# Kernel tuning notes

Measured on AMD Instinct MI355X. Metric: run time of the kernel, lower is better.

## Reference

```python
import jax, jax.numpy as jnp
import numpy as np

H = 1024      # LSTM_DIM
D = 1024      # BERT_DIM
VW = 30000    # word vocab
VA = 30       # action vocab
T = 64        # transition steps
S = 512       # BERT memory length


def lstm_cell(x, h, c, Wih, Whh, bih, bhh):
    # torch.nn.LSTMCell math: gates ordered i, f, g, o
    g = x @ Wih.T + bih + h @ Whh.T + bhh
    i, f, gg, o = jnp.split(g, 4, axis=-1)
    c2 = jax.nn.sigmoid(f) * c + jax.nn.sigmoid(i) * jnp.tanh(gg)
    h2 = jax.nn.sigmoid(o) * jnp.tanh(c2)
    return h2, c2


def forward(memory, actions, words,
            term_Wih, term_Whh, term_bih, term_bhh,
            act_Wih, act_Whh, act_bih, act_bhh,
            Wq, bq, Wa1, ba1, Wa2, ba2, Ww1, bw1, Ww2, bw2,
            act_emb, word_emb):
    z = jnp.zeros((1, H), dtype=memory.dtype)

    def step(carry, xs):
        term_h, term_c, act_h, act_c, stack_h = carry
        a_t, w_t = xs
        # predict_action: concat decoder states, dot-attention over BERT memory (no softmax)
        states = jnp.concatenate([term_h, act_h, stack_h], axis=1)     # [1, 3H]
        q = states @ Wq.T + bq                                          # [1, D]
        attn = jnp.einsum('bsd,bd->bs', memory, q)                      # [1, S]
        ctx = jnp.einsum('bs,bsd->bd', attn, memory)                    # [1, D]
        final = jnp.concatenate([states, ctx], axis=1)                  # [1, 3H+D]
        act_logits = jax.nn.relu(final @ Wa1.T + ba1) @ Wa2.T + ba2     # [1, VA]
        word_logits = jax.nn.relu(final @ Ww1.T + bw1) @ Ww2.T + bw2    # [1, VW]
        # do_action: act LSTM step, then SHIFT: word embedding into term LSTM + stack push
        a_e = act_emb[a_t][None, :]
        act_h2, act_c2 = lstm_cell(a_e, act_h, act_c, act_Wih, act_Whh, act_bih, act_bhh)
        w_e = word_emb[w_t][None, :]
        term_h2, term_c2 = lstm_cell(w_e, term_h, term_c, term_Wih, term_Whh, term_bih, term_bhh)
        new_carry = (term_h2, term_c2, act_h2, act_c2, w_e)
        return new_carry, (act_logits[0], word_logits[0])

    carry0 = (z, z, z, z, z)
    _, (act_logits, word_logits) = jax.lax.scan(step, carry0, (actions, words))
    return act_logits, word_logits  # [T, VA], [T, VW]


def setup_inputs() -> dict:
    key = jax.random.key(0)
    ks = jax.random.split(key, 24)
    s = 0.02

    def n(k, shape):
        return jax.random.normal(k, shape, dtype=jnp.float32) * s

    return {
        'memory': jax.random.normal(ks[0], (1, S, D), dtype=jnp.float32),
        'actions': jax.random.randint(ks[1], (T,), 0, VA),
        'words': jax.random.randint(ks[2], (T,), 0, VW),
        'term_Wih': n(ks[3], (4 * H, H)), 'term_Whh': n(ks[4], (4 * H, H)),
        'term_bih': n(ks[5], (4 * H,)), 'term_bhh': n(ks[6], (4 * H,)),
        'act_Wih': n(ks[7], (4 * H, H)), 'act_Whh': n(ks[8], (4 * H, H)),
        'act_bih': n(ks[9], (4 * H,)), 'act_bhh': n(ks[10], (4 * H,)),
        'Wq': n(ks[11], (D, 3 * H)), 'bq': n(ks[12], (D,)),
        'Wa1': n(ks[13], (H, 3 * H + D)), 'ba1': n(ks[14], (H,)),
        'Wa2': n(ks[15], (VA, H)), 'ba2': n(ks[16], (VA,)),
        'Ww1': n(ks[17], (H, 3 * H + D)), 'bw1': n(ks[18], (H,)),
        'Ww2': n(ks[19], (VW, H)), 'bw2': n(ks[20], (VW,)),
        'act_emb': n(ks[21], (VA, H)),
        'word_emb': n(ks[22], (VW, H)),
    }


def reference(memory, actions, words,
              term_Wih, term_Whh, term_bih, term_bhh,
              act_Wih, act_Whh, act_bih, act_bhh,
              Wq, bq, Wa1, ba1, Wa2, ba2, Ww1, bw1, Ww2, bw2,
              act_emb, word_emb):
    return forward(memory, actions, words,
                   term_Wih, term_Whh, term_bih, term_bhh,
                   act_Wih, act_Whh, act_bih, act_bhh,
                   Wq, bq, Wa1, ba1, Wa2, ba2, Ww1, bw1, Ww2, bw2,
                   act_emb, word_emb)
```

## Files before the change

kernel.cpp:

```cpp
#include <hip/hip_runtime.h>

#define H 1024
#define T_STEPS 64
#define S_MEM 512
#define VA 30
#define VW 30000

typedef unsigned long long u64;

__device__ __forceinline__ float sigmf(float x) { return 1.f / (1.f + expf(-x)); }

__global__ __launch_bounds__(256) void k_init(
    const int* __restrict__ actions, const int* __restrict__ words,
    const float* __restrict__ act_emb, const float* __restrict__ word_emb,
    float* __restrict__ X_term, float* __restrict__ X_act,
    float* __restrict__ fin, u64* __restrict__ htag) {
  int b = blockIdx.x, tid = threadIdx.x;
  if (b < T_STEPS) {
    int wi = words[b], ai = actions[b];
    for (int i = tid; i < H; i += 256) {
      float we = word_emb[(size_t)wi * H + i];
      X_term[b * H + i] = we;
      X_act[b * H + i]  = act_emb[(size_t)ai * H + i];
      if (b + 1 < T_STEPS) fin[(size_t)(b + 1) * 4096 + 2048 + i] = we;
    }
    if (b == 0)
      for (int i = tid; i < H; i += 256) fin[2048 + i] = 0.f;
  } else if (b == T_STEPS) {
    for (int i = tid; i < H; i += 256) { fin[i] = 0.f; fin[H + i] = 0.f; }
  } else {
    for (int i = (b - 65) * 256 + tid; i < 64 * 2048; i += 64 * 256) htag[i] = 0ull;
  }
}

__global__ __launch_bounds__(256) void k_gemm64(
    const float* __restrict__ A, int lda,
    const float* __restrict__ B, int ldb,
    int N, int K, float* __restrict__ Ppart) {
  __shared__ __align__(16) float As[64 * 64];
  __shared__ __align__(16) float Bs[64 * 64];
  const float4* As4 = (const float4*)As;
  const float4* Bs4 = (const float4*)Bs;
  int tid = threadIdx.x;
  int cidx = tid & 15;
  int ridx = tid >> 4;
  int n0 = blockIdx.x * 64;
  int klen = K / gridDim.y;
  int kbeg = blockIdx.y * klen;
  float acc[4][4] = {};

  for (int k0 = kbeg; k0 < kbeg + klen; k0 += 64) {
#pragma unroll
    for (int i = 0; i < 4; ++i) {
      int f = tid + i * 256;
      int rr = f >> 4, km = f & 15;
      float4 v = *(const float4*)&A[(size_t)rr * lda + k0 + km * 4];
      int c2 = ((rr >> 2) ^ km) & 15, p = rr & 3;
      As[(km * 4 + 0) * 64 + c2 * 4 + p] = v.x;
      As[(km * 4 + 1) * 64 + c2 * 4 + p] = v.y;
      As[(km * 4 + 2) * 64 + c2 * 4 + p] = v.z;
      As[(km * 4 + 3) * 64 + c2 * 4 + p] = v.w;
    }
#pragma unroll
    for (int i = 0; i < 4; ++i) {
      int f = tid + i * 256;
      int nn = f >> 4, km = f & 15;
      int gn = n0 + nn;
      float4 v = make_float4(0.f, 0.f, 0.f, 0.f);
      if (gn < N) v = *(const float4*)&B[(size_t)gn * ldb + k0 + km * 4];
      int c2 = ((nn >> 2) ^ km) & 15, p = nn & 3;
      Bs[(km * 4 + 0) * 64 + c2 * 4 + p] = v.x;
      Bs[(km * 4 + 1) * 64 + c2 * 4 + p] = v.y;
      Bs[(km * 4 + 2) * 64 + c2 * 4 + p] = v.z;
      Bs[(km * 4 + 3) * 64 + c2 * 4 + p] = v.w;
    }
    __syncthreads();
#pragma unroll 8
    for (int kk = 0; kk < 64; ++kk) {
      int sw = kk >> 2;
      float4 a4 = As4[kk * 16 + ((ridx ^ sw) & 15)];
      float4 b4 = Bs4[kk * 16 + ((cidx ^ sw) & 15)];
      float av[4] = {a4.x, a4.y, a4.z, a4.w};
      float bv[4] = {b4.x, b4.y, b4.z, b4.w};
#pragma unroll
      for (int i = 0; i < 4; ++i)
#pragma unroll
        for (int j = 0; j < 4; ++j) acc[i][j] += av[i] * bv[j];
    }
    __syncthreads();
  }

  int gcol = n0 + cidx * 4;
  float* P = Ppart + (size_t)blockIdx.y * 64 * N;
  if (gcol < N) {
#pragma unroll
    for (int i = 0; i < 4; ++i) {
      int row = ridx * 4 + i;
      *(float4*)&P[(size_t)row * N + gcol] =
          make_float4(acc[i][0], acc[i][1], acc[i][2], acc[i][3]);
    }
  }
}

__global__ __launch_bounds__(256) void k_gemm_dual(
    const float* __restrict__ A0, const float* __restrict__ A1, int lda,
    const float* __restrict__ B0, const float* __restrict__ B1, int ldb,
    int N, int K, float* __restrict__ P0, float* __restrict__ P1,
    const float* __restrict__ APc, int kb) {
  __shared__ __align__(16) float As[64 * 64];
  __shared__ __align__(16) float Bs[64 * 64];
  const float4* As4 = (const float4*)As;
  const float4* Bs4 = (const float4*)Bs;
  const float* A = blockIdx.z ? A1 : A0;
  const float* B = blockIdx.z ? B1 : B0;
  float* Pp = blockIdx.z ? P1 : P0;
  int tid = threadIdx.x;
  int cidx = tid & 15;
  int ridx = tid >> 4;
  int n0 = blockIdx.x * 64;
  int klen = K / gridDim.y;
  int kbeg = blockIdx.y * klen;
  float acc[4][4] = {};

  for (int k0 = kbeg; k0 < kbeg + klen; k0 += 64) {
#pragma unroll
    for (int i = 0; i < 4; ++i) {
      int f = tid + i * 256;
      int rr = f >> 4, km = f & 15;
      float4 v;
      if (k0 >= kb) {
        int kc = k0 - kb + km * 4;
        float4 a = *(const float4*)&APc[(size_t)rr * 1024 + kc];
        float4 c = *(const float4*)&APc[65536 + (size_t)rr * 1024 + kc];
        v = make_float4(a.x + c.x, a.y + c.y, a.z + c.z, a.w + c.w);
      } else {
        v = *(const float4*)&A[(size_t)rr * lda + k0 + km * 4];
      }
      int c2 = ((rr >> 2) ^ km) & 15, p = rr & 3;
      As[(km * 4 + 0) * 64 + c2 * 4 + p] = v.x;
      As[(km * 4 + 1) * 64 + c2 * 4 + p] = v.y;
      As[(km * 4 + 2) * 64 + c2 * 4 + p] = v.z;
      As[(km * 4 + 3) * 64 + c2 * 4 + p] = v.w;
    }
#pragma unroll
    for (int i = 0; i < 4; ++i) {
      int f = tid + i * 256;
      int nn = f >> 4, km = f & 15;
      int gn = n0 + nn;
      float4 v = make_float4(0.f, 0.f, 0.f, 0.f);
      if (gn < N) v = *(const float4*)&B[(size_t)gn * ldb + k0 + km * 4];
      int c2 = ((nn >> 2) ^ km) & 15, p = nn & 3;
      Bs[(km * 4 + 0) * 64 + c2 * 4 + p] = v.x;
      Bs[(km * 4 + 1) * 64 + c2 * 4 + p] = v.y;
      Bs[(km * 4 + 2) * 64 + c2 * 4 + p] = v.z;
      Bs[(km * 4 + 3) * 64 + c2 * 4 + p] = v.w;
    }
    __syncthreads();
#pragma unroll 8
    for (int kk = 0; kk < 64; ++kk) {
      int sw = kk >> 2;
      float4 a4 = As4[kk * 16 + ((ridx ^ sw) & 15)];
      float4 b4 = Bs4[kk * 16 + ((cidx ^ sw) & 15)];
      float av[4] = {a4.x, a4.y, a4.z, a4.w};
      float bv[4] = {b4.x, b4.y, b4.z, b4.w};
#pragma unroll
      for (int i = 0; i < 4; ++i)
#pragma unroll
        for (int j = 0; j < 4; ++j) acc[i][j] += av[i] * bv[j];
    }
    __syncthreads();
  }
  int gcol = n0 + cidx * 4;
  float* P = Pp + (size_t)blockIdx.y * 64 * N;
  if (gcol < N) {
#pragma unroll
    for (int i = 0; i < 4; ++i) {
      int row = ridx * 4 + i;
      *(float4*)&P[(size_t)row * N + gcol] =
          make_float4(acc[i][0], acc[i][1], acc[i][2], acc[i][3]);
    }
  }
}

__global__ __launch_bounds__(256) void k_attn(
    const float* __restrict__ Pq, const float* __restrict__ bq,
    const float* __restrict__ mem, float* __restrict__ Pa) {
  __shared__ __align__(16) float As[64 * 64];
  __shared__ __align__(16) float Bs[64 * 64];
  const float4* As4 = (const float4*)As;
  const float4* Bs4 = (const float4*)Bs;
  int tid = threadIdx.x;
  int cidx = tid & 15;
  int ridx = tid >> 4;
  int n0 = blockIdx.x * 64;
  int kbeg = blockIdx.y * 128;
  float acc[4][4] = {};

  for (int k0 = kbeg; k0 < kbeg + 128; k0 += 64) {
#pragma unroll
    for (int i = 0; i < 4; ++i) {
      int f = tid + i * 256;
      int rr = f >> 4, km = f & 15;
      int col = k0 + km * 4;
      float4 v = *(const float4*)&bq[col];
#pragma unroll
      for (int s = 0; s < 8; ++s) {
        float4 p = *(const float4*)&Pq[(size_t)s * 65536 + (size_t)rr * 1024 + col];
        v.x += p.x; v.y += p.y; v.z += p.z; v.w += p.w;
      }
      int c2 = ((rr >> 2) ^ km) & 15, p = rr & 3;
      As[(km * 4 + 0) * 64 + c2 * 4 + p] = v.x;
      As[(km * 4 + 1) * 64 + c2 * 4 + p] = v.y;
      As[(km * 4 + 2) * 64 + c2 * 4 + p] = v.z;
      As[(km * 4 + 3) * 64 + c2 * 4 + p] = v.w;
    }
#pragma unroll
    for (int i = 0; i < 4; ++i) {
      int f = tid + i * 256;
      int nn = f >> 4, km = f & 15;
      float4 v = *(const float4*)&mem[(size_t)(n0 + nn) * 1024 + k0 + km * 4];
      int c2 = ((nn >> 2) ^ km) & 15, p = nn & 3;
      Bs[(km * 4 + 0) * 64 + c2 * 4 + p] = v.x;
      Bs[(km * 4 + 1) * 64 + c2 * 4 + p] = v.y;
      Bs[(km * 4 + 2) * 64 + c2 * 4 + p] = v.z;
      Bs[(km * 4 + 3) * 64 + c2 * 4 + p] = v.w;
    }
    __syncthreads();
#pragma unroll 8
    for (int kk = 0; kk < 64; ++kk) {
      int sw = kk >> 2;
      float4 a4 = As4[kk * 16 + ((ridx ^ sw) & 15)];
      float4 b4 = Bs4[kk * 16 + ((cidx ^ sw) & 15)];
      float av[4] = {a4.x, a4.y, a4.z, a4.w};
      float bv[4] = {b4.x, b4.y, b4.z, b4.w};
#pragma unroll
      for (int i = 0; i < 4; ++i)
#pragma unroll
        for (int j = 0; j < 4; ++j) acc[i][j] += av[i] * bv[j];
    }
    __syncthreads();
  }
  int gcol = n0 + cidx * 4;
  float* P = Pa + (size_t)blockIdx.y * 64 * 512;
#pragma unroll
  for (int i = 0; i < 4; ++i) {
    int row = ridx * 4 + i;
    *(float4*)&P[(size_t)row * 512 + gcol] =
        make_float4(acc[i][0], acc[i][1], acc[i][2], acc[i][3]);
  }
}

__global__ __launch_bounds__(256) void k_ctx(
    const float* __restrict__ Pa, const float* __restrict__ mem,
    float* __restrict__ Pc) {
  __shared__ __align__(16) float As[64 * 64];
  __shared__ __align__(16) float Bs[64 * 64];
  const float4* As4 = (const float4*)As;
  const float4* Bs4 = (const float4*)Bs;
  int tid = threadIdx.x;
  int cidx = tid & 15;
  int ridx = tid >> 4;
  int n0 = blockIdx.x * 64;
  int kbeg = blockIdx.y * 256;
  float acc[4][4] = {};

  for (int k0 = kbeg; k0 < kbeg + 256; k0 += 64) {
#pragma unroll
    for (int i = 0; i < 4; ++i) {
      int f = tid + i * 256;
      int rr = f >> 4, km = f & 15;
      int col = k0 + km * 4;
      float4 v = make_float4(0.f, 0.f, 0.f, 0.f);
#pragma unroll
      for (int s = 0; s < 8; ++s) {
        float4 p = *(const float4*)&Pa[(size_t)s * 32768 + (size_t)rr * 512 + col];
        v.x += p.x; v.y += p.y; v.z += p.z; v.w += p.w;
      }
      int c2 = ((rr >> 2) ^ km) & 15, p = rr & 3;
      As[(km * 4 + 0) * 64 + c2 * 4 + p] = v.x;
      As[(km * 4 + 1) * 64 + c2 * 4 + p] = v.y;
      As[(km * 4 + 2) * 64 + c2 * 4 + p] = v.z;
      As[(km * 4 + 3) * 64 + c2 * 4 + p] = v.w;
    }
#pragma unroll
    for (int i = 0; i < 4; ++i) {
      int f = tid + i * 256;
      int kr = f >> 4, nq = f & 15;
      float4 v = *(const float4*)&mem[(size_t)(k0 + kr) * 1024 + n0 + nq * 4];
      ((float4*)Bs)[kr * 16 + ((nq ^ (kr >> 2)) & 15)] = v;
    }
    __syncthreads();
#pragma unroll 8
    for (int kk = 0; kk < 64; ++kk) {
      int sw = kk >> 2;
      float4 a4 = As4[kk * 16 + ((ridx ^ sw) & 15)];
      float4 b4 = Bs4[kk * 16 + ((cidx ^ sw) & 15)];
      float av[4] = {a4.x, a4.y, a4.z, a4.w};
      float bv[4] = {b4.x, b4.y, b4.z, b4.w};
#pragma unroll
      for (int i = 0; i < 4; ++i)
#pragma unroll
        for (int j = 0; j < 4; ++j) acc[i][j] += av[i] * bv[j];
    }
    __syncthreads();
  }
  int gcol = n0 + cidx * 4;
  float* P = Pc + (size_t)blockIdx.y * 64 * 1024;
#pragma unroll
  for (int i = 0; i < 4; ++i) {
    int row = ridx * 4 + i;
    *(float4*)&P[(size_t)row * 1024 + gcol] =
        make_float4(acc[i][0], acc[i][1], acc[i][2], acc[i][3]);
  }
}

__global__ __launch_bounds__(256) void k_reduce_dual(
    const float* __restrict__ P0, const float* __restrict__ P1, int S, int N,
    const float* __restrict__ ba0, const float* __restrict__ ba1,
    float* __restrict__ o0, float* __restrict__ o1, int relu) {
  const float* P = blockIdx.y ? P1 : P0;
  const float* bias = blockIdx.y ? ba1 : ba0;
  float* out = blockIdx.y ? o1 : o0;
  int q = blockIdx.x * 256 + threadIdx.x;
  int total = 64 * N / 4;
  if (q >= total) return;
  int e0 = q * 4;
  int col = e0 % N;
  float4 v = make_float4(0, 0, 0, 0);
  for (int s = 0; s < S; ++s) {
    float4 p = *(const float4*)&P[(size_t)s * 64 * N + e0];
    v.x += p.x; v.y += p.y; v.z += p.z; v.w += p.w;
  }
  if (bias) {
    float4 b = *(const float4*)&bias[col];
    v.x += b.x; v.y += b.y; v.z += b.z; v.w += b.w;
  }
  if (relu) {
    v.x = fmaxf(v.x, 0.f); v.y = fmaxf(v.y, 0.f);
    v.z = fmaxf(v.z, 0.f); v.w = fmaxf(v.w, 0.f);
  }
  *(float4*)&out[e0] = v;
}

__global__ __launch_bounds__(256) void k_reduce4(
    const float* __restrict__ P, int S, int N,
    const float* __restrict__ bias, float* __restrict__ out) {
  int q = blockIdx.x * 256 + threadIdx.x;
  int total = 64 * N / 4;
  if (q >= total) return;
  int e0 = q * 4;
  int col = e0 % N;
  float4 v = make_float4(0, 0, 0, 0);
  for (int s = 0; s < S; ++s) {
    float4 p = *(const float4*)&P[(size_t)s * 64 * N + e0];
    v.x += p.x; v.y += p.y; v.z += p.z; v.w += p.w;
  }
  float4 b = *(const float4*)&bias[col];
  v.x += b.x; v.y += b.y; v.z += b.z; v.w += b.w;
  *(float4*)&out[e0] = v;
}

__global__ __launch_bounds__(256, 1) void k_recur(
    const float* __restrict__ Whh_term, const float* __restrict__ Whh_act,
    const float* __restrict__ Pxg_term, const float* __restrict__ Pxg_act,
    const float* __restrict__ bih_t, const float* __restrict__ bhh_t,
    const float* __restrict__ bih_a, const float* __restrict__ bhh_a,
    float* __restrict__ fin, u64* __restrict__ htag) {
  __shared__ float hs[32 * 36];
  __shared__ float xgs[63 * 32];
  int b = blockIdx.x, tid = threadIdx.x;
  int lstm = b >> 7, k0 = (b & 127) * 8;
  const float* Whh = lstm ? Whh_act : Whh_term;
  const float* Pxg = lstm ? Pxg_act : Pxg_term;
  const float* bih = lstm ? bih_a : bih_t;
  const float* bhh = lstm ? bhh_a : bhh_t;
  int d = tid >> 5, p = tid & 31;

  float wreg[128];
#pragma unroll
  for (int g = 0; g < 4; ++g) {
    const float* wrow = Whh + (size_t)(g * 1024 + k0 + d) * 1024 + p * 32;
#pragma unroll
    for (int i = 0; i < 32; i += 4) {
      float4 v = *(const float4*)(wrow + i);
      wreg[g * 32 + i]     = v.x; wreg[g * 32 + i + 1] = v.y;
      wreg[g * 32 + i + 2] = v.z; wreg[g * 32 + i + 3] = v.w;
    }
  }
#pragma unroll
  for (int i = 0; i < 128; ++i) asm volatile("" : "+v"(wreg[i]));

  for (int i = tid; i < 63 * 32; i += 256) {
    int rr = i & 31, t2 = i >> 5;
    int row2 = (rr >> 3) * 1024 + k0 + (rr & 7);
    xgs[i] = Pxg[(size_t)t2 * 4096 + row2] + Pxg[262144 + (size_t)t2 * 4096 + row2] +
             bih[row2] + bhh[row2];
  }
  float c_loc = 0.f;

  for (int t = 0; t < 63; ++t) {
    if (t > 0) {
      const u64* src = htag + (size_t)t * 2048 + lstm * 1024;
      u64 v0 = __hip_atomic_load(&src[tid], __ATOMIC_RELAXED, __HIP_MEMORY_SCOPE_AGENT);
      u64 v1 = __hip_atomic_load(&src[tid + 256], __ATOMIC_RELAXED, __HIP_MEMORY_SCOPE_AGENT);
      u64 v2 = __hip_atomic_load(&src[tid + 512], __ATOMIC_RELAXED, __HIP_MEMORY_SCOPE_AGENT);
      u64 v3 = __hip_atomic_load(&src[tid + 768], __ATOMIC_RELAXED, __HIP_MEMORY_SCOPE_AGENT);
      while ((unsigned)(v0 >> 32) != (unsigned)t) {
        __builtin_amdgcn_s_sleep(1);
        v0 = __hip_atomic_load(&src[tid], __ATOMIC_RELAXED, __HIP_MEMORY_SCOPE_AGENT);
      }
      while ((unsigned)(v1 >> 32) != (unsigned)t) {
        __builtin_amdgcn_s_sleep(1);
        v1 = __hip_atomic_load(&src[tid + 256], __ATOMIC_RELAXED, __HIP_MEMORY_SCOPE_AGENT);
      }
      while ((unsigned)(v2 >> 32) != (unsigned)t) {
        __builtin_amdgcn_s_sleep(1);
        v2 = __hip_atomic_load(&src[tid + 512], __ATOMIC_RELAXED, __HIP_MEMORY_SCOPE_AGENT);
      }
      while ((unsigned)(v3 >> 32) != (unsigned)t) {
        __builtin_amdgcn_s_sleep(1);
        v3 = __hip_atomic_load(&src[tid + 768], __ATOMIC_RELAXED, __HIP_MEMORY_SCOPE_AGENT);
      }
      hs[((tid) >> 5) * 36 + (tid & 31)]         = __uint_as_float((unsigned)v0);
      hs[((tid + 256) >> 5) * 36 + (tid & 31)]   = __uint_as_float((unsigned)v1);
      hs[((tid + 512) >> 5) * 36 + (tid & 31)]   = __uint_as_float((unsigned)v2);
      hs[((tid + 768) >> 5) * 36 + (tid & 31)]   = __uint_as_float((unsigned)v3);
    } else {
#pragma unroll
      for (int j = 0; j < 4; ++j) {
        int idx = tid + j * 256;
        hs[(idx >> 5) * 36 + (idx & 31)] = 0.f;
      }
    }
    __syncthreads();

    const float* hp = hs + p * 36;
    float s0 = 0.f, s1 = 0.f, s2 = 0.f, s3 = 0.f;
#pragma unroll
    for (int i = 0; i < 32; i += 4) {
      float4 hv = *(const float4*)&hp[i];
      s0 += wreg[i] * hv.x + wreg[i + 1] * hv.y + wreg[i + 2] * hv.z + wreg[i + 3] * hv.w;
      s1 += wreg[32 + i] * hv.x + wreg[33 + i] * hv.y + wreg[34 + i] * hv.z + wreg[35 + i] * hv.w;
      s2 += wreg[64 + i] * hv.x + wreg[65 + i] * hv.y + wreg[66 + i] * hv.z + wreg[67 + i] * hv.w;
      s3 += wreg[96 + i] * hv.x + wreg[97 + i] * hv.y + wreg[98 + i] * hv.z + wreg[99 + i] * hv.w;
    }
#pragma unroll
    for (int m = 1; m <= 16; m <<= 1) {
      s0 += __shfl_xor(s0, m); s1 += __shfl_xor(s1, m);
      s2 += __shfl_xor(s2, m); s3 += __shfl_xor(s3, m);
    }
    if (p == 0) {
      float gi = s0 + xgs[t * 32 + d];
      float gf = s1 + xgs[t * 32 + 8 + d];
      float gg = s2 + xgs[t * 32 + 16 + d];
      float go = s3 + xgs[t * 32 + 24 + d];
      float c2 = sigmf(gf) * c_loc + sigmf(gi) * tanhf(gg);
      float h2 = sigmf(go) * tanhf(c2);
      c_loc = c2;
      fin[(size_t)(t + 1) * 4096 + lstm * 1024 + k0 + d] = h2;
      __hip_atomic_store(&htag[(size_t)(t + 1) * 2048 + lstm * 1024 + k0 + d],
                         (((u64)(t + 1)) << 32) | (u64)__float_as_uint(h2),
                         __ATOMIC_RELAXED, __HIP_MEMORY_SCOPE_AGENT);
    }
    __syncthreads();
  }
}

__global__ __launch_bounds__(256) void k_wordN(
    const float* __restrict__ hw, const float* __restrict__ Ww2,
    const float* __restrict__ bw2, float* __restrict__ Pword,
    float* __restrict__ outw) {
  __shared__ __align__(16) float As[64 * 64];
  __shared__ __align__(16) float Bs0[64 * 64];
  __shared__ __align__(16) float Bs1[64 * 64];
  const float4* As4  = (const float4*)As;
  const float4* Bs04 = (const float4*)Bs0;
  const float4* Bs14 = (const float4*)Bs1;
  int tid = threadIdx.x;
  int cidx = tid & 15;
  int ridx = tid >> 4;
  int n0 = blockIdx.x * 128;
  int splitk = gridDim.y;
  int klen = 1024 / splitk;
  int kbeg = blockIdx.y * klen;
  float acc0[4][4] = {}, acc1[4][4] = {};

  for (int k0 = kbeg; k0 < kbeg + klen; k0 += 64) {
#pragma unroll
    for (int i = 0; i < 4; ++i) {
      int f = tid + i * 256;
      int rr = f >> 4, km = f & 15;
      float4 v = *(const float4*)&hw[(size_t)rr * 1024 + k0 + km * 4];
      int c2 = ((rr >> 2) ^ km) & 15, p = rr & 3;
      As[(km * 4 + 0) * 64 + c2 * 4 + p] = v.x;
      As[(km * 4 + 1) * 64 + c2 * 4 + p] = v.y;
      As[(km * 4 + 2) * 64 + c2 * 4 + p] = v.z;
      As[(km * 4 + 3) * 64 + c2 * 4 + p] = v.w;
    }
#pragma unroll
    for (int h = 0; h < 2; ++h) {
      float* Bsh = h ? Bs1 : Bs0;
#pragma unroll
      for (int i = 0; i < 4; ++i) {
        int f = tid + i * 256;
        int nn = f >> 4, km = f & 15;
        int gn = n0 + h * 64 + nn;
        float4 v = make_float4(0.f, 0.f, 0.f, 0.f);
        if (gn < VW) v = *(const float4*)&Ww2[(size_t)gn * 1024 + k0 + km * 4];
        int c2 = ((nn >> 2) ^ km) & 15, p = nn & 3;
        Bsh[(km * 4 + 0) * 64 + c2 * 4 + p] = v.x;
        Bsh[(km * 4 + 1) * 64 + c2 * 4 + p] = v.y;
        Bsh[(km * 4 + 2) * 64 + c2 * 4 + p] = v.z;
        Bsh[(km * 4 + 3) * 64 + c2 * 4 + p] = v.w;
      }
    }
    __syncthreads();
#pragma unroll 4
    for (int kk = 0; kk < 64; ++kk) {
      int sw = kk >> 2;
      float4 a4 = As4[kk * 16 + ((ridx ^ sw) & 15)];
      float4 b0 = Bs04[kk * 16 + ((cidx ^ sw) & 15)];
      float4 b1 = Bs14[kk * 16 + ((cidx ^ sw) & 15)];
      float av[4] = {a4.x, a4.y, a4.z, a4.w};
      float b0v[4] = {b0.x, b0.y, b0.z, b0.w};
      float b1v[4] = {b1.x, b1.y, b1.z, b1.w};
#pragma unroll
      for (int i = 0; i < 4; ++i)
#pragma unroll
        for (int j = 0; j < 4; ++j) {
          acc0[i][j] += av[i] * b0v[j];
          acc1[i][j] += av[i] * b1v[j];
        }
    }
    __syncthreads();
  }

  int g0 = n0 + cidx * 4;
  int g1 = n0 + 64 + cidx * 4;
  if (splitk > 1) {
    float* P = Pword + (size_t)blockIdx.y * 64 * VW;
#pragma unroll
    for (int i = 0; i < 4; ++i) {
      int row = ridx * 4 + i;
      if (g0 < VW)
        *(float4*)&P[(size_t)row * VW + g0] =
            make_float4(acc0[i][0], acc0[i][1], acc0[i][2], acc0[i][3]);
      if (g1 < VW)
        *(float4*)&P[(size_t)row * VW + g1] =
            make_float4(acc1[i][0], acc1[i][1], acc1[i][2], acc1[i][3]);
    }
  } else {
#pragma unroll
    for (int i = 0; i < 4; ++i) {
      int row = ridx * 4 + i;
      if (g0 < VW) {
        float4 b = *(const float4*)&bw2[g0];
        *(float4*)&outw[(size_t)row * VW + g0] =
            make_float4(acc0[i][0] + b.x, acc0[i][1] + b.y,
                        acc0[i][2] + b.z, acc0[i][3] + b.w);
      }
      if (g1 < VW) {
        float4 b = *(const float4*)&bw2[g1];
        *(float4*)&outw[(size_t)row * VW + g1] =
            make_float4(acc1[i][0] + b.x, acc1[i][1] + b.y,
                        acc1[i][2] + b.z, acc1[i][3] + b.w);
      }
    }
  }
}

__global__ __launch_bounds__(256) void k_actlog(
    const float* __restrict__ ha, const float* __restrict__ Wa2,
    const float* __restrict__ ba2, float* __restrict__ out) {
  int t = blockIdx.x, tid = threadIdx.x;
  int v = tid >> 3, p = tid & 7;
  float sum = 0.f;
  if (v < VA) {
    const float* a  = ha + (size_t)t * 1024 + p * 128;
    const float* wr = Wa2 + (size_t)v * 1024 + p * 128;
#pragma unroll 8
    for (int i = 0; i < 128; i += 4) {
      float4 av = *(const float4*)(a + i);
      float4 wv = *(const float4*)(wr + i);
      sum += av.x * wv.x + av.y * wv.y + av.z * wv.z + av.w * wv.w;
    }
  }
  sum += __shfl_xor(sum, 1);
  sum += __shfl_xor(sum, 2);
  sum += __shfl_xor(sum, 4);
  if (p == 0 && v < VA) out[(size_t)t * VA + v] = sum + ba2[v];
}

extern "C" void kernel_launch(void* const* d_in, const int* in_sizes, int n_in,
                              void* d_out, int out_size, void* d_ws, size_t ws_size,
                              hipStream_t stream) {
  const float* memory   = (const float*)d_in[0];
  const int*   actions  = (const int*)d_in[1];
  const int*   words    = (const int*)d_in[2];
  const float* term_Wih = (const float*)d_in[3];
  const float* term_Whh = (const float*)d_in[4];
  const float* term_bih = (const float*)d_in[5];
  const float* term_bhh = (const float*)d_in[6];
  const float* act_Wih  = (const float*)d_in[7];
  const float* act_Whh  = (const float*)d_in[8];
  const float* act_bih  = (const float*)d_in[9];
  const float* act_bhh  = (const float*)d_in[10];
  const float* Wq  = (const float*)d_in[11];
  const float* bq  = (const float*)d_in[12];
  const float* Wa1 = (const float*)d_in[13];
  const float* ba1 = (const float*)d_in[14];
  const float* Wa2 = (const float*)d_in[15];
  const float* ba2 = (const float*)d_in[16];
  const float* Ww1 = (const float*)d_in[17];
  const float* bw1 = (const float*)d_in[18];
  const float* Ww2 = (const float*)d_in[19];
  const float* bw2 = (const float*)d_in[20];
  const float* act_emb  = (const float*)d_in[21];
  const float* word_emb = (const float*)d_in[22];
  float* out = (float*)d_out;

  float* w      = (float*)d_ws;
  float* fin    = w;
  u64*   htag   = (u64*)(w + 262144);
  float* Pa     = (float*)htag;
  float* X_term = w + 524288;
  float* X_act  = w + 589824;
  float* Pc     = X_term;
  float* ha     = w + 655360;
  float* hw     = w + 720896;
  float* arena  = w + 786432;

  int wsplit = (ws_size >= (size_t)(786432 + 4ull * 64 * VW) * 4) ? 4
             : (ws_size >= (size_t)(786432 + 2ull * 64 * VW) * 4) ? 2 : 1;

  k_init<<<129, 256, 0, stream>>>(actions, words, act_emb, word_emb,
                                  X_term, X_act, fin, htag);

  k_gemm_dual<<<dim3(64, 2, 2), 256, 0, stream>>>(
      X_term, X_act, 1024, term_Wih, act_Wih, 1024, 4096, 1024,
      arena, arena + 524288, nullptr, 1 << 30);

  k_recur<<<256, 256, 0, stream>>>(term_Whh, act_Whh, arena, arena + 524288,
                                   term_bih, term_bhh, act_bih, act_bhh, fin, htag);

  k_gemm64<<<dim3(16, 8), 256, 0, stream>>>(fin, 4096, Wq, 3072, 1024, 3072, arena);

  k_attn<<<dim3(8, 8), 256, 0, stream>>>(arena, bq, memory, Pa);

  k_ctx<<<dim3(16, 2), 256, 0, stream>>>(Pa, memory, Pc);

  k_gemm_dual<<<dim3(16, 8, 2), 256, 0, stream>>>(
      fin, fin, 4096, Wa1, Ww1, 4096, 1024, 4096,
      arena, arena + 524288, Pc, 3072);
  k_reduce_dual<<<dim3(64, 2), 256, 0, stream>>>(
      arena, arena + 524288, 8, 1024, ba1, bw1, ha, hw, 1);

  k_actlog<<<64, 256, 0, stream>>>(ha, Wa2, ba2, out);

  k_wordN<<<dim3(235, wsplit), 256, 0, stream>>>(hw, Ww2, bw2, arena, out + 1920);
  if (wsplit > 1)
    k_reduce4<<<1875, 256, 0, stream>>>(arena, wsplit, VW, bw2, out + 1920);
}
```

Measured before the change: 485.4 us.

## Use bf16 MFMA for word projection with weight conversion overlapped in recurrence

The fp32 split-K word-logit GEMM (64x30000x1024) is replaced by a bf16 MFMA kernel. The Ww2 fp32-to-bf16 conversion runs in extra blocks of the latency-bound recurrence kernel, so it overlaps with the serial LSTM phase, and the ReLU'd hidden states are packed to bf16 in the reduce kernel. The recurrence also double-buffers its shared h buffer so the trailing barrier can be dropped. This trades fp32 accuracy for bf16 inputs, and the conversion runs on every call, which adds about 180MB of memory traffic.

```diff
diff --git a/kernel.cpp b/kernel.cpp
--- a/kernel.cpp
+++ b/kernel.cpp
@@ -5,10 +5,17 @@
 #define S_MEM 512
 #define VA 30
 #define VW 30000
+#define VWPAD 30016
 
 typedef unsigned long long u64;
+typedef __attribute__((ext_vector_type(8))) short short8;
+typedef __attribute__((ext_vector_type(4))) float f32x4;
 
 __device__ __forceinline__ float sigmf(float x) { return 1.f / (1.f + expf(-x)); }
+__device__ __forceinline__ unsigned short f2bf(float f) {
+  unsigned u = __float_as_uint(f);
+  return (unsigned short)((u + 0x7FFFu + ((u >> 16) & 1u)) >> 16);
+}
 
 __global__ __launch_bounds__(256) void k_init(
     const int* __restrict__ actions, const int* __restrict__ words,
@@ -317,7 +324,8 @@
 __global__ __launch_bounds__(256) void k_reduce_dual(
     const float* __restrict__ P0, const float* __restrict__ P1, int S, int N,
     const float* __restrict__ ba0, const float* __restrict__ ba1,
-    float* __restrict__ o0, float* __restrict__ o1, int relu) {
+    float* __restrict__ o0, float* __restrict__ o1, int relu,
+    unsigned short* __restrict__ hwb_out) {
   const float* P = blockIdx.y ? P1 : P0;
   const float* bias = blockIdx.y ? ba1 : ba0;
   float* out = blockIdx.y ? o1 : o0;
@@ -340,6 +348,11 @@
     v.z = fmaxf(v.z, 0.f); v.w = fmaxf(v.w, 0.f);
   }
   *(float4*)&out[e0] = v;
+  if (blockIdx.y == 1 && hwb_out) {
+    unsigned pk0 = (unsigned)f2bf(v.x) | ((unsigned)f2bf(v.y) << 16);
+    unsigned pk1 = (unsigned)f2bf(v.z) | ((unsigned)f2bf(v.w) << 16);
+    *(uint2*)&hwb_out[e0] = make_uint2(pk0, pk1);
+  }
 }
 
 __global__ __launch_bounds__(256) void k_reduce4(
@@ -365,10 +378,32 @@
     const float* __restrict__ Pxg_term, const float* __restrict__ Pxg_act,
     const float* __restrict__ bih_t, const float* __restrict__ bhh_t,
     const float* __restrict__ bih_a, const float* __restrict__ bhh_a,
-    float* __restrict__ fin, u64* __restrict__ htag) {
-  __shared__ float hs[32 * 36];
+    float* __restrict__ fin, u64* __restrict__ htag,
+    const float* __restrict__ Ww2src, unsigned short* __restrict__ ww2b) {
+  int b = blockIdx.x, tid = threadIdx.x;
+  if (b >= 256) {
+    if (!ww2b) return;
+    const size_t E  = (size_t)VWPAD * 1024;
+    const size_t VE = (size_t)VW * 1024;
+    size_t stride = (size_t)(gridDim.x - 256) * 256 * 8;
+    for (size_t idx = ((size_t)(b - 256) * 256 + tid) * 8; idx < E; idx += stride) {
+      unsigned pk[4];
+      if (idx + 8 <= VE) {
+        float4 f0 = *(const float4*)&Ww2src[idx];
+        float4 f1 = *(const float4*)&Ww2src[idx + 4];
+        pk[0] = (unsigned)f2bf(f0.x) | ((unsigned)f2bf(f0.y) << 16);
+        pk[1] = (unsigned)f2bf(f0.z) | ((unsigned)f2bf(f0.w) << 16);
+        pk[2] = (unsigned)f2bf(f1.x) | ((unsigned)f2bf(f1.y) << 16);
+        pk[3] = (unsigned)f2bf(f1.z) | ((unsigned)f2bf(f1.w) << 16);
+      } else {
+        pk[0] = pk[1] = pk[2] = pk[3] = 0u;
+      }
+      *(uint4*)&ww2b[idx] = make_uint4(pk[0], pk[1], pk[2], pk[3]);
+    }
+    return;
+  }
+  __shared__ float hs[2][32 * 36];
   __shared__ float xgs[63 * 32];
-  int b = blockIdx.x, tid = threadIdx.x;
   int lstm = b >> 7, k0 = (b & 127) * 8;
   const float* Whh = lstm ? Whh_act : Whh_term;
   const float* Pxg = lstm ? Pxg_act : Pxg_term;
@@ -399,6 +434,7 @@
   float c_loc = 0.f;
 
   for (int t = 0; t < 63; ++t) {
+    float* hb = hs[t & 1];
     if (t > 0) {
       const u64* src = htag + (size_t)t * 2048 + lstm * 1024;
       u64 v0 = __hip_atomic_load(&src[tid], __ATOMIC_RELAXED, __HIP_MEMORY_SCOPE_AGENT);
@@ -421,20 +457,20 @@
         __builtin_amdgcn_s_sleep(1);
         v3 = __hip_atomic_load(&src[tid + 768], __ATOMIC_RELAXED, __HIP_MEMORY_SCOPE_AGENT);
       }
-      hs[((tid) >> 5) * 36 + (tid & 31)]         = __uint_as_float((unsigned)v0);
-      hs[((tid + 256) >> 5) * 36 + (tid & 31)]   = __uint_as_float((unsigned)v1);
-      hs[((tid + 512) >> 5) * 36 + (tid & 31)]   = __uint_as_float((unsigned)v2);
-      hs[((tid + 768) >> 5) * 36 + (tid & 31)]   = __uint_as_float((unsigned)v3);
+      hb[((tid) >> 5) * 36 + (tid & 31)]         = __uint_as_float((unsigned)v0);
+      hb[((tid + 256) >> 5) * 36 + (tid & 31)]   = __uint_as_float((unsigned)v1);
+      hb[((tid + 512) >> 5) * 36 + (tid & 31)]   = __uint_as_float((unsigned)v2);
+      hb[((tid + 768) >> 5) * 36 + (tid & 31)]   = __uint_as_float((unsigned)v3);
     } else {
 #pragma unroll
       for (int j = 0; j < 4; ++j) {
         int idx = tid + j * 256;
-        hs[(idx >> 5) * 36 + (idx & 31)] = 0.f;
-      }
-    }
-    __syncthreads();
-
-    const float* hp = hs + p * 36;
+        hb[(idx >> 5) * 36 + (idx & 31)] = 0.f;
+      }
+    }
+    __syncthreads();
+
+    const float* hp = hb + p * 36;
     float s0 = 0.f, s1 = 0.f, s2 = 0.f, s3 = 0.f;
 #pragma unroll
     for (int i = 0; i < 32; i += 4) {
@@ -462,7 +498,52 @@
                          (((u64)(t + 1)) << 32) | (u64)__float_as_uint(h2),
                          __ATOMIC_RELAXED, __HIP_MEMORY_SCOPE_AGENT);
     }
-    __syncthreads();
+  }
+}
+
+__global__ __launch_bounds__(256) void k_word_mfma(
+    const unsigned short* __restrict__ hwb, const unsigned short* __restrict__ ww2b,
+    const float* __restrict__ bw2, float* __restrict__ outw) {
+  int tid = threadIdx.x;
+  int wv = tid >> 6, lane = tid & 63;
+  int col = blockIdx.x * 64 + wv * 16 + (lane & 15);
+  int kg = (lane >> 4) * 8;
+  const unsigned short* brow = ww2b + (size_t)col * 1024 + kg;
+  const unsigned short* arow = hwb + (size_t)(lane & 15) * 1024 + kg;
+  f32x4 acc0 = {0.f, 0.f, 0.f, 0.f}, acc1 = acc0, acc2 = acc0, acc3 = acc0;
+
+  short8 bf = *(const short8*)brow;
+  short8 a0 = *(const short8*)(arow);
+  short8 a1 = *(const short8*)(arow + 16 * 1024);
+  short8 a2 = *(const short8*)(arow + 32 * 1024);
+  short8 a3 = *(const short8*)(arow + 48 * 1024);
+  for (int k0 = 0; k0 < 992; k0 += 32) {
+    short8 bf_n = *(const short8*)(brow + k0 + 32);
+    short8 a0n = *(const short8*)(arow + k0 + 32);
+    short8 a1n = *(const short8*)(arow + 16 * 1024 + k0 + 32);
+    short8 a2n = *(const short8*)(arow + 32 * 1024 + k0 + 32);
+    short8 a3n = *(const short8*)(arow + 48 * 1024 + k0 + 32);
+    acc0 = __builtin_amdgcn_mfma_f32_16x16x32_bf16(a0, bf, acc0, 0, 0, 0);
+    acc1 = __builtin_amdgcn_mfma_f32_16x16x32_bf16(a1, bf, acc1, 0, 0, 0);
+    acc2 = __builtin_amdgcn_mfma_f32_16x16x32_bf16(a2, bf, acc2, 0, 0, 0);
+    acc3 = __builtin_amdgcn_mfma_f32_16x16x32_bf16(a3, bf, acc3, 0, 0, 0);
+    bf = bf_n; a0 = a0n; a1 = a1n; a2 = a2n; a3 = a3n;
+  }
+  acc0 = __builtin_amdgcn_mfma_f32_16x16x32_bf16(a0, bf, acc0, 0, 0, 0);
+  acc1 = __builtin_amdgcn_mfma_f32_16x16x32_bf16(a1, bf, acc1, 0, 0, 0);
+  acc2 = __builtin_amdgcn_mfma_f32_16x16x32_bf16(a2, bf, acc2, 0, 0, 0);
+  acc3 = __builtin_amdgcn_mfma_f32_16x16x32_bf16(a3, bf, acc3, 0, 0, 0);
+
+  if (col < VW) {
+    float bias = bw2[col];
+    int r0 = (lane >> 4) * 4;
+#pragma unroll
+    for (int j = 0; j < 4; ++j) {
+      outw[(size_t)(r0 + j) * VW + col]      = acc0[j] + bias;
+      outw[(size_t)(16 + r0 + j) * VW + col] = acc1[j] + bias;
+      outw[(size_t)(32 + r0 + j) * VW + col] = acc2[j] + bias;
+      outw[(size_t)(48 + r0 + j) * VW + col] = acc3[j] + bias;
+    }
   }
 }
 
@@ -629,7 +710,11 @@
   float* ha     = w + 655360;
   float* hw     = w + 720896;
   float* arena  = w + 786432;
-
+  unsigned short* ww2b = (unsigned short*)(arena + 1048576);
+  unsigned short* hwb  = (unsigned short*)(arena + 1048576 + 15368192);
+
+  size_t need_bf16 = (size_t)(786432 + 1048576 + 15368192 + 32768) * 4;
+  bool bf16w = ws_size >= need_bf16;
   int wsplit = (ws_size >= (size_t)(786432 + 4ull * 64 * VW) * 4) ? 4
              : (ws_size >= (size_t)(786432 + 2ull * 64 * VW) * 4) ? 2 : 1;
 
@@ -640,8 +725,10 @@
       X_term, X_act, 1024, term_Wih, act_Wih, 1024, 4096, 1024,
       arena, arena + 524288, nullptr, 1 << 30);
 
-  k_recur<<<256, 256, 0, stream>>>(term_Whh, act_Whh, arena, arena + 524288,
-                                   term_bih, term_bhh, act_bih, act_bhh, fin, htag);
+  k_recur<<<bf16w ? 960 : 256, 256, 0, stream>>>(
+      term_Whh, act_Whh, arena, arena + 524288,
+      term_bih, term_bhh, act_bih, act_bhh, fin, htag,
+      Ww2, bf16w ? ww2b : nullptr);
 
   k_gemm64<<<dim3(16, 8), 256, 0, stream>>>(fin, 4096, Wq, 3072, 1024, 3072, arena);
 
@@ -653,11 +740,16 @@
       fin, fin, 4096, Wa1, Ww1, 4096, 1024, 4096,
       arena, arena + 524288, Pc, 3072);
   k_reduce_dual<<<dim3(64, 2), 256, 0, stream>>>(
-      arena, arena + 524288, 8, 1024, ba1, bw1, ha, hw, 1);
+      arena, arena + 524288, 8, 1024, ba1, bw1, ha, hw, 1,
+      bf16w ? hwb : nullptr);
 
   k_actlog<<<64, 256, 0, stream>>>(ha, Wa2, ba2, out);
 
-  k_wordN<<<dim3(235, wsplit), 256, 0, stream>>>(hw, Ww2, bw2, arena, out + 1920);
-  if (wsplit > 1)
-    k_reduce4<<<1875, 256, 0, stream>>>(arena, wsplit, VW, bw2, out + 1920);
-}
+  if (bf16w) {
+    k_word_mfma<<<469, 256, 0, stream>>>(hwb, ww2b, bw2, out + 1920);
+  } else {
+    k_wordN<<<dim3(235, wsplit), 256, 0, stream>>>(hw, Ww2, bw2, arena, out + 1920);
+    if (wsplit > 1)
+      k_reduce4<<<1875, 256, 0, stream>>>(arena, wsplit, VW, bw2, out + 1920);
+  }
+}
```

New measurement: 485.7 us. About the same (+0.1%).
